# Performance work log

Hardware: AMD Instinct MI355X
Metric: run time of the kernel (lower is better)

## Reference

```python
import jax, jax.numpy as jnp
import numpy as np

N_SRC = 50000
N_DST = 50000
N_EDGES = 1_600_000
D_NEIGH = 128
D_SELF = 128
D_EDGE = 32
D_OUT = 256


def setup_inputs() -> dict:
    key = jax.random.key(0)
    k = jax.random.split(key, 7)
    h_neigh = jax.random.normal(k[0], (N_SRC, D_NEIGH), dtype=jnp.float32)
    h_self = jax.random.normal(k[1], (N_DST, D_SELF), dtype=jnp.float32)
    edge_feats = jax.random.normal(k[2], (N_EDGES, D_EDGE), dtype=jnp.float32)
    src = jax.random.randint(k[3], (N_EDGES,), 0, N_SRC, dtype=jnp.int32)
    dst = jax.random.randint(k[4], (N_EDGES,), 0, N_DST, dtype=jnp.int32)
    # xavier-ish small weights
    W_self = jax.random.normal(k[5], (D_OUT, D_SELF), dtype=jnp.float32) * 0.05
    W_neigh = jax.random.normal(k[6], (D_OUT, D_NEIGH + D_EDGE), dtype=jnp.float32) * 0.05
    return {"h_neigh": h_neigh, "h_self": h_self, "edge_feats": edge_feats,
            "src": src, "dst": dst, "W_self": W_self, "W_neigh": W_neigh}


def reference(h_neigh, h_self, edge_feats, src, dst, W_self, W_neigh):
    n_dst = h_self.shape[0]
    # in-degree per destination node (mean denominator); zero-degree -> 0 result like DGL
    deg = jax.ops.segment_sum(jnp.ones_like(dst, dtype=h_neigh.dtype), dst, num_segments=n_dst)
    denom = jnp.where(deg == 0, 1.0, deg)[:, None]
    # fn.copy_e + mean: mean of edge features per destination node
    edge_agg = jax.ops.segment_sum(edge_feats, dst, num_segments=n_dst) / denom  # [n_dst, D_EDGE]
    # fn.copy_u + mean: gather neighbor features along edges, mean-scatter to dst
    neigh_agg = jax.ops.segment_sum(h_neigh[src], dst, num_segments=n_dst) / denom  # [n_dst, D_NEIGH]
    hn = jnp.concatenate([neigh_agg, edge_agg], axis=1)  # [n_dst, D_NEIGH+D_EDGE]
    z = jax.nn.relu(h_self @ W_self.T + hn @ W_neigh.T)  # [n_dst, D_OUT]
    z_norm = jnp.linalg.norm(z, ord=2, axis=1, keepdims=True)
    z_norm = jnp.where(z_norm == 0, 1.0, z_norm)
    return z / z_norm
```

## Files before the change

kernel.cpp:

```cpp
#include <hip/hip_runtime.h>

#define N_SRC 50000
#define N_DST 50000
#define N_EDGES 1600000
#define D_NEIGH 128
#define D_SELF 128
#define D_EDGE 32
#define D_OUT 256
#define K_TOT 288
#define D_HN 160

#define NB 196
#define CPAD 16
#define CHUNK 2048
#define CAPSH 14
#define NSCAT1 256

typedef float f32x4 __attribute__((ext_vector_type(4)));
typedef short s16x8 __attribute__((ext_vector_type(8)));
typedef float fv4 __attribute__((ext_vector_type(4)));
typedef float fv2 __attribute__((ext_vector_type(2)));
typedef unsigned short uv4 __attribute__((ext_vector_type(4)));

__device__ __forceinline__ ushort f2bf(float x) {
    unsigned b = __float_as_uint(x);
    return (ushort)((b + 0x7fffu + ((b >> 16) & 1u)) >> 16);
}
__device__ __forceinline__ float bflo(unsigned u) { return __uint_as_float(u << 16); }
__device__ __forceinline__ float bfhi(unsigned u) { return __uint_as_float(u & 0xffff0000u); }


#if defined(__has_builtin)
#if __has_builtin(__builtin_amdgcn_cvt_pk_fp8_f32) && __has_builtin(__builtin_amdgcn_cvt_pk_f32_fp8)
#define FP8_HW 1
#endif
#endif

__device__ __forceinline__ unsigned enc_fp8_scalar(float x) {
    unsigned b = __float_as_uint(x);
    const unsigned s = b >> 31;
    float ax = fabsf(x);
    ax = fminf(ax, 448.f);
    if (ax < 0.015625f) return s << 7;
    unsigned ab = __float_as_uint(ax);
    unsigned lsb = (ab >> 20) & 1u;
    unsigned b2 = ab + 0x7FFFFu + lsb;
    unsigned e = ((b2 >> 23) & 0xFFu) - 120u;
    unsigned m = (b2 >> 20) & 7u;
    if (e > 15u) { e = 15u; m = 6u; }
    return (s << 7) | (e << 3) | m;
}

__device__ __forceinline__ unsigned enc_fp8x4(float4 f) {
#ifdef FP8_HW
    int r = 0;
    r = __builtin_amdgcn_cvt_pk_fp8_f32(f.x, f.y, r, false);
    r = __builtin_amdgcn_cvt_pk_fp8_f32(f.z, f.w, r, true);
    return (unsigned)r;
#else
    return enc_fp8_scalar(f.x) | (enc_fp8_scalar(f.y) << 8) |
           (enc_fp8_scalar(f.z) << 16) | (enc_fp8_scalar(f.w) << 24);
#endif
}

__device__ __forceinline__ float dec_fp8_scalar(unsigned u) {
    unsigned e = (u >> 3) & 15u;
    unsigned bits = ((u & 0x80u) << 24) | (((u & 0x7Fu) << 20) + (120u << 23));
    return (e == 0) ? 0.f : __uint_as_float(bits);
}

__device__ __forceinline__ void dec_fp8x4(unsigned u, float* f) {
#ifdef FP8_HW
    fv2 lo = __builtin_amdgcn_cvt_pk_f32_fp8(u, false);
    fv2 hi = __builtin_amdgcn_cvt_pk_f32_fp8(u, true);
    f[0] = lo.x; f[1] = lo.y; f[2] = hi.x; f[3] = hi.y;
#else
    f[0] = dec_fp8_scalar(u);
    f[1] = dec_fp8_scalar(u >> 8);
    f[2] = dec_fp8_scalar(u >> 16);
    f[3] = dec_fp8_scalar(u >> 24);
#endif
}


__global__ __launch_bounds__(256) void k_pre(const int* __restrict__ dst,
                                             const int* __restrict__ src,
                                             int* __restrict__ gcur0,
                                             int2* __restrict__ pk1,
                                             const float* __restrict__ h_neigh,
                                             unsigned* __restrict__ hb,
                                             const float* __restrict__ Wself,
                                             const float* __restrict__ Wneigh,
                                             ushort* __restrict__ Wb) {
    __shared__ int hist[NB];
    __shared__ int lbase[NB];
    __shared__ int gbase[NB];
    __shared__ int2 stage[CHUNK];
    const int blk = blockIdx.x;
    const int tid = threadIdx.x;

    if (blk >= NSCAT1) {
        const int bb = blk - NSCAT1;
        if (bb < 6250) {
            const int i = bb * 256 + tid;
            float4 f = ((const float4*)h_neigh)[i];
            hb[i] = enc_fp8x4(f);
        } else {
            const int q = (bb - 6250) * 256 + tid;
            if (q >= 9 * 4 * 256) return;
            const int t = q >> 10;
            const int r = q & 1023;
            const int k8 = r >> 8;
            const int c = r & 255;
            const int kb = t * 32 + k8 * 8;
            const float* p = (kb < 128) ? (Wself + (size_t)c * D_SELF + kb)
                                        : (Wneigh + (size_t)c * D_HN + (kb - 128));
            float4 f0 = *(const float4*)(p);
            float4 f1 = *(const float4*)(p + 4);
            ushort* o = Wb + (size_t)q * 8;
            *(ushort4*)(o)     = make_ushort4(f2bf(f0.x), f2bf(f0.y), f2bf(f0.z), f2bf(f0.w));
            *(ushort4*)(o + 4) = make_ushort4(f2bf(f1.x), f2bf(f1.y), f2bf(f1.z), f2bf(f1.w));
        }
        return;
    }

    const int n = N_EDGES;
    for (int c0 = blk * CHUNK; c0 < n; c0 += NSCAT1 * CHUNK) {
        const int m = min(CHUNK, n - c0);
        for (int t = tid; t < NB; t += 256) hist[t] = 0;
        __syncthreads();
        int d8[8], s8[8];
#pragma unroll
        for (int j = 0; j < 8; j++) {
            const int i = c0 + j * 256 + tid;
            if (i < n) { d8[j] = dst[i]; s8[j] = src[i]; atomicAdd(&hist[d8[j] >> 8], 1); }
        }
        __syncthreads();
        if (tid == 0) {
            int ex = 0;
            for (int b = 0; b < NB; b++) { lbase[b] = ex; ex += hist[b]; }
        }
        __syncthreads();
        for (int t = tid; t < NB; t += 256)
            gbase[t] = hist[t] ? atomicAdd(&gcur0[t * CPAD], hist[t]) : 0;
        __syncthreads();
        for (int t = tid; t < NB; t += 256) hist[t] = lbase[t];
        __syncthreads();
#pragma unroll
        for (int j = 0; j < 8; j++) {
            const int i = c0 + j * 256 + tid;
            if (i < n) {
                const unsigned cb = (unsigned)d8[j] >> 8;
                const int p = atomicAdd(&hist[cb], 1);
                stage[p] = make_int2(i, (int)((unsigned)s8[j] |
                                              (((unsigned)d8[j] & 255u) << 16) | (cb << 24)));
            }
        }
        __syncthreads();
        for (int t = tid; t < m; t += 256) {
            int2 v = stage[t];
            const int cb = (v.y >> 24) & 255;
            v.y &= 0x00FFFFFF;
            pk1[((size_t)cb << CAPSH) + gbase[cb] + (t - lbase[cb])] = v;
        }
        __syncthreads();
    }
}


__global__ __launch_bounds__(1024) void k_scat2(const int* __restrict__ gcur0,
                                                const int2* __restrict__ pk1,
                                                int2* __restrict__ pk2,
                                                int2* __restrict__ rs2) {
    __shared__ int part[256];
    __shared__ int cur[256];
    const int b = blockIdx.x;
    const int n = gcur0[b * CPAD];
    const int base = b << CAPSH;
    const int tid = threadIdx.x;
    if (tid < 256) part[tid] = 0;
    __syncthreads();
    for (int i = tid; i < n; i += 1024)
        atomicAdd(&part[(pk1[base + i].y >> 16) & 255], 1);
    __syncthreads();
    const int c0 = (tid < 256) ? part[tid] : 0;
    __syncthreads();
    for (int off = 1; off < 256; off <<= 1) {
        int v = 0;
        if (tid < 256 && tid >= off) v = part[tid - off];
        __syncthreads();
        if (tid < 256) part[tid] += v;
        __syncthreads();
    }
    if (tid < 256) {
        const int pfx = part[tid] - c0;
        cur[tid] = pfx;
        const int gn = b * 256 + tid;
        if (gn < N_DST) rs2[gn] = make_int2(base + pfx, base + pfx + c0);
    }
    __syncthreads();
    for (int i = tid; i < n; i += 1024) {
        int2 v = pk1[base + i];
        const int dl = (v.y >> 16) & 255;
        const int p = atomicAdd(&cur[dl], 1);
        pk2[base + p] = make_int2(v.x, v.y & 0xFFFF);
    }
}


__global__ void k_cvtall(const float* __restrict__ in, unsigned* __restrict__ hb,
                         const float* __restrict__ Wself, const float* __restrict__ Wneigh,
                         ushort* __restrict__ Wb) {
    const int b = blockIdx.x;
    if (b < 6250) {
        const int i = b * 256 + threadIdx.x;
        float4 f = ((const float4*)in)[i];
        hb[i] = enc_fp8x4(f);
    } else {
        const int q = (b - 6250) * 256 + threadIdx.x;
        if (q >= 9 * 4 * 256) return;
        const int t = q >> 10;
        const int r = q & 1023;
        const int k8 = r >> 8;
        const int c = r & 255;
        const int kb = t * 32 + k8 * 8;
        const float* p = (kb < 128) ? (Wself + (size_t)c * D_SELF + kb)
                                    : (Wneigh + (size_t)c * D_HN + (kb - 128));
        float4 f0 = *(const float4*)(p);
        float4 f1 = *(const float4*)(p + 4);
        ushort* o = Wb + (size_t)q * 8;
        *(ushort4*)(o)     = make_ushort4(f2bf(f0.x), f2bf(f0.y), f2bf(f0.z), f2bf(f0.w));
        *(ushort4*)(o + 4) = make_ushort4(f2bf(f1.x), f2bf(f1.y), f2bf(f1.z), f2bf(f1.w));
    }
}

__global__ void k_deg(const int* __restrict__ dst, int* __restrict__ deg, int n) {
    int i = blockIdx.x * blockDim.x + threadIdx.x;
    if (i < n) atomicAdd(&deg[dst[i]], 1);
}

__global__ __launch_bounds__(1024) void k_scan(const int* __restrict__ deg,
                                               int* __restrict__ row_start,
                                               int* __restrict__ cursor) {
    __shared__ int part[1024];
    const int t = threadIdx.x;
    const int CH = (N_DST + 1023) / 1024;
    const int b = t * CH;
    int s = 0;
    for (int i = 0; i < CH; i++) { int idx = b + i; if (idx < N_DST) s += deg[idx]; }
    part[t] = s;
    __syncthreads();
    for (int off = 1; off < 1024; off <<= 1) {
        int v = (t >= off) ? part[t - off] : 0;
        __syncthreads();
        part[t] += v;
        __syncthreads();
    }
    int ex = (t == 0) ? 0 : part[t - 1];
    for (int i = 0; i < CH; i++) {
        int idx = b + i;
        if (idx < N_DST) { row_start[idx] = ex; cursor[idx] = ex; ex += deg[idx]; }
    }
    if (t == 1023) row_start[N_DST] = part[1023];
}

__global__ void k_fill(const int* __restrict__ dst, const int* __restrict__ src,
                       int* __restrict__ cursor, int2* __restrict__ pk, int n) {
    int i = blockIdx.x * blockDim.x + threadIdx.x;
    if (i < n) {
        int p = atomicAdd(&cursor[dst[i]], 1);
        pk[p] = make_int2(i, src[i]);
    }
}

__global__ void k_mkrs2(const int* __restrict__ row_start, int2* __restrict__ rs2) {
    int i = blockIdx.x * blockDim.x + threadIdx.x;
    if (i < N_DST) rs2[i] = make_int2(row_start[i], row_start[i + 1]);
}


__global__ __launch_bounds__(64) void k_agg(const int2* __restrict__ rs2,
                                            const int2* __restrict__ pk,
                                            const unsigned char* __restrict__ hb,
                                            const float* __restrict__ ef,
                                            ushort* __restrict__ hnb) {
    const int d = blockIdx.x;
    const int lane = threadIdx.x;
    const int ll = lane & 31;
    const int g = lane >> 5;
    const int2 se = rs2[d];
    const int start = se.x, end = se.y;
    const int deg = end - start;
    float a0 = 0.f, a1 = 0.f, a2 = 0.f, a3 = 0.f, ae = 0.f;
    const unsigned char* hbase = hb + 4 * ll;
    const float* ebase = ef + ll;

    for (int c = start; c < end; c += 64) {
        const int rem = end - c;
        const int m = rem < 64 ? rem : 64;
        int e = 0, s = 0;
        if (lane < m) {
            unsigned long long pv =
                __builtin_nontemporal_load((const unsigned long long*)&pk[c + lane]);
            e = (int)(unsigned)pv;
            s = (int)(unsigned)(pv >> 32);
        }
        int i = 0;
        for (; i + 16 <= m; i += 16) {
            unsigned u[8];
            float te[8];
#pragma unroll
            for (int j = 0; j < 8; j++) {
                const int sj = __shfl(s, i + 2 * j + g);
                u[j] = *(const unsigned*)(hbase + (size_t)sj * D_NEIGH);
            }
#pragma unroll
            for (int j = 0; j < 8; j++) {
                const int ee = __shfl(e, i + 2 * j + g);
                te[j] = __builtin_nontemporal_load(ebase + (size_t)ee * D_EDGE);
            }
#pragma unroll
            for (int j = 0; j < 8; j++) {
                float f[4];
                dec_fp8x4(u[j], f);
                a0 += f[0]; a1 += f[1]; a2 += f[2]; a3 += f[3];
                ae += te[j];
            }
        }
        for (; i + 8 <= m; i += 8) {
            unsigned u[4];
            float te[4];
#pragma unroll
            for (int j = 0; j < 4; j++) {
                const int sj = __shfl(s, i + 2 * j + g);
                u[j] = *(const unsigned*)(hbase + (size_t)sj * D_NEIGH);
            }
#pragma unroll
            for (int j = 0; j < 4; j++) {
                const int ee = __shfl(e, i + 2 * j + g);
                te[j] = __builtin_nontemporal_load(ebase + (size_t)ee * D_EDGE);
            }
#pragma unroll
            for (int j = 0; j < 4; j++) {
                float f[4];
                dec_fp8x4(u[j], f);
                a0 += f[0]; a1 += f[1]; a2 += f[2]; a3 += f[3];
                ae += te[j];
            }
        }
        for (; i < m; ++i) {
            const int si = __builtin_amdgcn_readlane(s, i);
            const int ei = __builtin_amdgcn_readlane(e, i);
            if (g == 0) {
                const unsigned uu = *(const unsigned*)(hbase + (size_t)si * D_NEIGH);
                float f[4];
                dec_fp8x4(uu, f);
                a0 += f[0]; a1 += f[1]; a2 += f[2]; a3 += f[3];
                ae += __builtin_nontemporal_load(ebase + (size_t)ei * D_EDGE);
            }
        }
    }

    a0 += __shfl_xor(a0, 32); a1 += __shfl_xor(a1, 32);
    a2 += __shfl_xor(a2, 32); a3 += __shfl_xor(a3, 32);
    ae += __shfl_xor(ae, 32);

    if (lane < 32) {
        const float inv = 1.0f / (float)(deg > 0 ? deg : 1);
        ushort* o = hnb + (size_t)d * D_HN;
        *(ushort4*)(o + 4 * ll) = make_ushort4(f2bf(a0 * inv), f2bf(a1 * inv),
                                               f2bf(a2 * inv), f2bf(a3 * inv));
        o[128 + ll] = f2bf(ae * inv);
    }
}


#define GBM 128

__global__ __launch_bounds__(512) void k_gemm_norm(const float* __restrict__ h_self,
                                                   const ushort* __restrict__ hnb,
                                                   const ushort* __restrict__ Wb,
                                                   float* __restrict__ out) {
    __shared__ __align__(16) ushort Xs[2][GBM * 40];
    __shared__ float rsum[2][GBM];
    __shared__ float invn[GBM];

    const int tid = threadIdx.x;
    const int lane = tid & 63;
    const int wid = tid >> 6;
    const int wm = wid >> 1;
    const int wn = wid & 1;
    const int brow = blockIdx.x * GBM;
    const int xrow = tid >> 2, xpart = tid & 3;
    const int koff8 = lane >> 4, rsel = lane & 15;

    f32x4 acc[2][8] = {};

    auto stageX = [&](int t, int bufi) {
        const int k0 = t * 32;
        const int gr = brow + xrow;
        uv4 v0 = (uv4)0, v1 = (uv4)0;
        if (gr < N_DST) {
            if (k0 < 128) {
                const float* sp = h_self + (size_t)gr * D_SELF + k0 + xpart * 8;
                fv4 f0 = __builtin_nontemporal_load((const fv4*)(sp));
                fv4 f1 = __builtin_nontemporal_load((const fv4*)(sp + 4));
                v0 = (uv4){f2bf(f0.x), f2bf(f0.y), f2bf(f0.z), f2bf(f0.w)};
                v1 = (uv4){f2bf(f1.x), f2bf(f1.y), f2bf(f1.z), f2bf(f1.w)};
            } else {
                const ushort* sp = hnb + (size_t)gr * D_HN + (k0 - 128) + xpart * 8;
                v0 = __builtin_nontemporal_load((const uv4*)(sp));
                v1 = __builtin_nontemporal_load((const uv4*)(sp + 4));
            }
        }
        *(uv4*)&Xs[bufi][xrow * 40 + xpart * 8] = v0;
        *(uv4*)&Xs[bufi][xrow * 40 + xpart * 8 + 4] = v1;
    };

    stageX(0, 0);
    __syncthreads();

    for (int t = 0; t < 9; t++) {
        if (t < 8) stageX(t + 1, (t + 1) & 1);
        s16x8 af[2], bf[8];
#pragma unroll
        for (int fi = 0; fi < 2; fi++)
            af[fi] = *(const s16x8*)&Xs[t & 1][(wm * 32 + fi * 16 + rsel) * 40 + koff8 * 8];
#pragma unroll
        for (int fj = 0; fj < 8; fj++)
            bf[fj] = *(const s16x8*)&Wb[((size_t)(t * 4 + koff8) * 256 +
                                         (wn * 128 + fj * 16 + rsel)) * 8];
#pragma unroll
        for (int fi = 0; fi < 2; fi++)
#pragma unroll
            for (int fj = 0; fj < 8; fj++)
                acc[fi][fj] = __builtin_amdgcn_mfma_f32_16x16x32_bf16(af[fi], bf[fj], acc[fi][fj], 0, 0, 0);
        __syncthreads();
    }

    float ss[2][4];
#pragma unroll
    for (int fi = 0; fi < 2; fi++)
#pragma unroll
        for (int j = 0; j < 4; j++) {
            float s = 0.f;
#pragma unroll
            for (int fj = 0; fj < 8; fj++) {
                float z = fmaxf(acc[fi][fj][j], 0.f);
                acc[fi][fj][j] = z;
                s += z * z;
            }
            ss[fi][j] = s;
        }
#pragma unroll
    for (int m = 1; m < 16; m <<= 1)
#pragma unroll
        for (int fi = 0; fi < 2; fi++)
#pragma unroll
            for (int j = 0; j < 4; j++) ss[fi][j] += __shfl_xor(ss[fi][j], m);
    if ((lane & 15) == 0) {
        const int gg = lane >> 4;
#pragma unroll
        for (int fi = 0; fi < 2; fi++)
#pragma unroll
            for (int j = 0; j < 4; j++)
                rsum[wn][wm * 32 + fi * 16 + gg * 4 + j] = ss[fi][j];
    }
    __syncthreads();
    if (tid < GBM) {
        float t = rsum[0][tid] + rsum[1][tid];
        invn[tid] = (t > 0.f) ? 1.f / sqrtf(t) : 1.f;
    }
    __syncthreads();

#pragma unroll
    for (int fi = 0; fi < 2; fi++)
#pragma unroll
        for (int j = 0; j < 4; j++) {
            const int rl = wm * 32 + fi * 16 + (lane >> 4) * 4 + j;
            const int row = brow + rl;
            if (row < N_DST) {
                const float iv = invn[rl];
#pragma unroll
                for (int fj = 0; fj < 8; fj++)
                    __builtin_nontemporal_store(acc[fi][fj][j] * iv,
                        &out[(size_t)row * D_OUT + wn * 128 + fj * 16 + (lane & 15)]);
            }
        }
}


extern "C" void kernel_launch(void* const* d_in, const int* in_sizes, int n_in,
                              void* d_out, int out_size, void* d_ws, size_t ws_size,
                              hipStream_t stream) {
    const float* h_neigh = (const float*)d_in[0];
    const float* h_self  = (const float*)d_in[1];
    const float* ef      = (const float*)d_in[2];
    const int*   src     = (const int*)d_in[3];
    const int*   dst     = (const int*)d_in[4];
    const float* Wself   = (const float*)d_in[5];
    const float* Wneigh  = (const float*)d_in[6];
    float* out = (float*)d_out;

    char* ws = (char*)d_ws;
    const size_t PKB = (size_t)NB << CAPSH;
    const size_t need_new = 524288ull + 2 * PKB * 8 + 12800000ull + 16000000ull + 147456ull;

    if (ws_size >= need_new) {
        int*   gcur0 = (int*)(ws + 0);
        int2*  rs2   = (int2*)(ws + 16384);
        int2*  pk1   = (int2*)(ws + 524288);
        int2*  pk2   = (int2*)(ws + 524288 + PKB * 8);
        unsigned* hb = (unsigned*)(ws + 524288 + 2 * PKB * 8);
        ushort* hnb  = (ushort*)((char*)hb + 12800000);
        ushort* Wb   = (ushort*)((char*)hnb + 16000000);

        hipMemsetAsync(gcur0, 0, NB * CPAD * sizeof(int), stream);
        k_pre<<<NSCAT1 + 6250 + 36, 256, 0, stream>>>(dst, src, gcur0, pk1,
                                                      h_neigh, hb, Wself, Wneigh, Wb);
        k_scat2<<<NB, 1024, 0, stream>>>(gcur0, pk1, pk2, rs2);
        k_agg<<<N_DST, 64, 0, stream>>>(rs2, pk2, (const unsigned char*)hb, ef, hnb);
        k_gemm_norm<<<(N_DST + GBM - 1) / GBM, 512, 0, stream>>>(h_self, hnb, Wb, out);
    } else {
        int* deg       = (int*)(ws + 0);
        int* row_start = (int*)(ws + 262144);
        int* cursor    = (int*)(ws + 524288);
        int2* pk       = (int2*)(ws + 786432);
        unsigned* hb   = (unsigned*)(ws + 13586432);
        ushort* hnb    = (ushort*)(ws + 26386432);
        ushort* Wb     = (ushort*)(ws + 42386432);
        int2* rs2      = (int2*)(ws + 42533888);

        hipMemsetAsync(deg, 0, N_DST * sizeof(int), stream);
        k_cvtall<<<6286, 256, 0, stream>>>(h_neigh, hb, Wself, Wneigh, Wb);
        k_deg<<<(N_EDGES + 255) / 256, 256, 0, stream>>>(dst, deg, N_EDGES);
        k_scan<<<1, 1024, 0, stream>>>(deg, row_start, cursor);
        k_fill<<<(N_EDGES + 255) / 256, 256, 0, stream>>>(dst, src, cursor, pk, N_EDGES);
        k_mkrs2<<<(N_DST + 255) / 256, 256, 0, stream>>>(row_start, rs2);
        k_agg<<<N_DST, 64, 0, stream>>>(rs2, pk, (const unsigned char*)hb, ef, hnb);
        k_gemm_norm<<<(N_DST + GBM - 1) / GBM, 512, 0, stream>>>(h_self, hnb, Wb, out);
    }
}
```

Before: 151.1 us.

## Fuse second scatter pass into aggregation with 64-node buckets sorted in LDS

After: 163.8 us. +8.4%, slower.

```diff
diff --git a/kernel.cpp b/kernel.cpp
--- a/kernel.cpp
+++ b/kernel.cpp
@@ -10,10 +10,10 @@
 #define K_TOT 288
 #define D_HN 160
 
-#define NB 196
+#define NBF 782
 #define CPAD 16
 #define CHUNK 2048
-#define CAPSH 14
+#define CAPSH 12
 #define NSCAT1 256
 
 typedef float f32x4 __attribute__((ext_vector_type(4)));
@@ -26,8 +26,6 @@
     unsigned b = __float_as_uint(x);
     return (ushort)((b + 0x7fffu + ((b >> 16) & 1u)) >> 16);
 }
-__device__ __forceinline__ float bflo(unsigned u) { return __uint_as_float(u << 16); }
-__device__ __forceinline__ float bfhi(unsigned u) { return __uint_as_float(u & 0xffff0000u); }
 
 
 #if defined(__has_builtin)
@@ -89,12 +87,15 @@
                                              int2* __restrict__ pk1,
                                              const float* __restrict__ h_neigh,
                                              unsigned* __restrict__ hb,
+                                             const float* __restrict__ h_self,
+                                             ushort* __restrict__ hsb,
                                              const float* __restrict__ Wself,
                                              const float* __restrict__ Wneigh,
                                              ushort* __restrict__ Wb) {
-    __shared__ int hist[NB];
-    __shared__ int lbase[NB];
-    __shared__ int gbase[NB];
+    __shared__ int hist[NBF];
+    __shared__ int lbase[NBF];
+    __shared__ int gbase[NBF];
+    __shared__ int partial[256];
     __shared__ int2 stage[CHUNK];
     const int blk = blockIdx.x;
     const int tid = threadIdx.x;
@@ -105,8 +106,12 @@
             const int i = bb * 256 + tid;
             float4 f = ((const float4*)h_neigh)[i];
             hb[i] = enc_fp8x4(f);
+        } else if (bb < 12500) {
+            const int i = (bb - 6250) * 256 + tid;
+            float4 f = ((const float4*)h_self)[i];
+            ((ushort4*)hsb)[i] = make_ushort4(f2bf(f.x), f2bf(f.y), f2bf(f.z), f2bf(f.w));
         } else {
-            const int q = (bb - 6250) * 256 + tid;
+            const int q = (bb - 12500) * 256 + tid;
             if (q >= 9 * 4 * 256) return;
             const int t = q >> 10;
             const int r = q & 1023;
@@ -127,40 +132,58 @@
     const int n = N_EDGES;
     for (int c0 = blk * CHUNK; c0 < n; c0 += NSCAT1 * CHUNK) {
         const int m = min(CHUNK, n - c0);
-        for (int t = tid; t < NB; t += 256) hist[t] = 0;
+        for (int t = tid; t < NBF; t += 256) hist[t] = 0;
         __syncthreads();
         int d8[8], s8[8];
 #pragma unroll
         for (int j = 0; j < 8; j++) {
             const int i = c0 + j * 256 + tid;
-            if (i < n) { d8[j] = dst[i]; s8[j] = src[i]; atomicAdd(&hist[d8[j] >> 8], 1); }
-        }
-        __syncthreads();
-        if (tid == 0) {
-            int ex = 0;
-            for (int b = 0; b < NB; b++) { lbase[b] = ex; ex += hist[b]; }
-        }
-        __syncthreads();
-        for (int t = tid; t < NB; t += 256)
+            if (i < n) { d8[j] = dst[i]; s8[j] = src[i]; atomicAdd(&hist[d8[j] >> 6], 1); }
+        }
+        __syncthreads();
+        int loc[4];
+        int sum = 0;
+#pragma unroll
+        for (int j = 0; j < 4; j++) {
+            const int bi = tid * 4 + j;
+            loc[j] = (bi < NBF) ? hist[bi] : 0;
+            sum += loc[j];
+        }
+        partial[tid] = sum;
+        __syncthreads();
+        for (int off = 1; off < 256; off <<= 1) {
+            int v = (tid >= off) ? partial[tid - off] : 0;
+            __syncthreads();
+            partial[tid] += v;
+            __syncthreads();
+        }
+        int ex = (tid == 0) ? 0 : partial[tid - 1];
+#pragma unroll
+        for (int j = 0; j < 4; j++) {
+            const int bi = tid * 4 + j;
+            if (bi < NBF) { lbase[bi] = ex; ex += loc[j]; }
+        }
+        __syncthreads();
+        for (int t = tid; t < NBF; t += 256)
             gbase[t] = hist[t] ? atomicAdd(&gcur0[t * CPAD], hist[t]) : 0;
         __syncthreads();
-        for (int t = tid; t < NB; t += 256) hist[t] = lbase[t];
+        for (int t = tid; t < NBF; t += 256) hist[t] = lbase[t];
         __syncthreads();
 #pragma unroll
         for (int j = 0; j < 8; j++) {
             const int i = c0 + j * 256 + tid;
             if (i < n) {
-                const unsigned cb = (unsigned)d8[j] >> 8;
+                const unsigned cb = (unsigned)d8[j] >> 6;
                 const int p = atomicAdd(&hist[cb], 1);
                 stage[p] = make_int2(i, (int)((unsigned)s8[j] |
-                                              (((unsigned)d8[j] & 255u) << 16) | (cb << 24)));
+                                              (((unsigned)d8[j] & 63u) << 16) | (cb << 22)));
             }
         }
         __syncthreads();
         for (int t = tid; t < m; t += 256) {
             int2 v = stage[t];
-            const int cb = (v.y >> 24) & 255;
-            v.y &= 0x00FFFFFF;
+            const unsigned cb = ((unsigned)v.y >> 22) & 1023u;
+            v.y &= 0x3FFFFF;
             pk1[((size_t)cb << CAPSH) + gbase[cb] + (t - lbase[cb])] = v;
         }
         __syncthreads();
@@ -168,216 +191,151 @@
 }
 
 
-__global__ __launch_bounds__(1024) void k_scat2(const int* __restrict__ gcur0,
-                                                const int2* __restrict__ pk1,
-                                                int2* __restrict__ pk2,
-                                                int2* __restrict__ rs2) {
-    __shared__ int part[256];
-    __shared__ int cur[256];
+__global__ __launch_bounds__(512) void k_aggs2(const int* __restrict__ gcur0,
+                                               const int2* __restrict__ pk1,
+                                               const unsigned char* __restrict__ hb,
+                                               const float* __restrict__ ef,
+                                               ushort* __restrict__ hnb) {
+    __shared__ int2 sorted[1 << CAPSH];
+    __shared__ int h[64];
+    __shared__ int sbase[65];
+    __shared__ int cur[64];
     const int b = blockIdx.x;
-    const int n = gcur0[b * CPAD];
-    const int base = b << CAPSH;
     const int tid = threadIdx.x;
-    if (tid < 256) part[tid] = 0;
-    __syncthreads();
-    for (int i = tid; i < n; i += 1024)
-        atomicAdd(&part[(pk1[base + i].y >> 16) & 255], 1);
-    __syncthreads();
-    const int c0 = (tid < 256) ? part[tid] : 0;
-    __syncthreads();
-    for (int off = 1; off < 256; off <<= 1) {
-        int v = 0;
-        if (tid < 256 && tid >= off) v = part[tid - off];
-        __syncthreads();
-        if (tid < 256) part[tid] += v;
-        __syncthreads();
-    }
-    if (tid < 256) {
-        const int pfx = part[tid] - c0;
-        cur[tid] = pfx;
-        const int gn = b * 256 + tid;
-        if (gn < N_DST) rs2[gn] = make_int2(base + pfx, base + pfx + c0);
-    }
-    __syncthreads();
-    for (int i = tid; i < n; i += 1024) {
-        int2 v = pk1[base + i];
-        const int dl = (v.y >> 16) & 255;
+    const int lane = tid & 63;
+    const int wid = tid >> 6;
+    const int nn = min(gcur0[b * CPAD], 1 << CAPSH);
+    const size_t base = (size_t)b << CAPSH;
+
+    if (tid < 64) h[tid] = 0;
+    __syncthreads();
+
+    int2 ent[8];
+    int ne = 0;
+#pragma unroll
+    for (int j = 0; j < 8; j++) {
+        const int idx = j * 512 + tid;
+        if (idx < nn) {
+            unsigned long long pv =
+                __builtin_nontemporal_load((const unsigned long long*)&pk1[base + idx]);
+            ent[ne].x = (int)(unsigned)pv;
+            ent[ne].y = (int)(unsigned)(pv >> 32);
+            atomicAdd(&h[(ent[ne].y >> 16) & 63], 1);
+            ne++;
+        }
+    }
+    __syncthreads();
+    if (tid < 64) {
+        const int v = h[tid];
+        int p = v;
+#pragma unroll
+        for (int off = 1; off < 64; off <<= 1) {
+            int q = __shfl_up(p, off);
+            if (lane >= off) p += q;
+        }
+        sbase[tid + 1] = p;
+        if (tid == 0) sbase[0] = 0;
+        cur[tid] = p - v;
+    }
+    __syncthreads();
+    for (int j = 0; j < ne; j++) {
+        const int dl = (ent[j].y >> 16) & 63;
         const int p = atomicAdd(&cur[dl], 1);
-        pk2[base + p] = make_int2(v.x, v.y & 0xFFFF);
-    }
-}
-
-
-__global__ void k_cvtall(const float* __restrict__ in, unsigned* __restrict__ hb,
-                         const float* __restrict__ Wself, const float* __restrict__ Wneigh,
-                         ushort* __restrict__ Wb) {
-    const int b = blockIdx.x;
-    if (b < 6250) {
-        const int i = b * 256 + threadIdx.x;
-        float4 f = ((const float4*)in)[i];
-        hb[i] = enc_fp8x4(f);
-    } else {
-        const int q = (b - 6250) * 256 + threadIdx.x;
-        if (q >= 9 * 4 * 256) return;
-        const int t = q >> 10;
-        const int r = q & 1023;
-        const int k8 = r >> 8;
-        const int c = r & 255;
-        const int kb = t * 32 + k8 * 8;
-        const float* p = (kb < 128) ? (Wself + (size_t)c * D_SELF + kb)
-                                    : (Wneigh + (size_t)c * D_HN + (kb - 128));
-        float4 f0 = *(const float4*)(p);
-        float4 f1 = *(const float4*)(p + 4);
-        ushort* o = Wb + (size_t)q * 8;
-        *(ushort4*)(o)     = make_ushort4(f2bf(f0.x), f2bf(f0.y), f2bf(f0.z), f2bf(f0.w));
-        *(ushort4*)(o + 4) = make_ushort4(f2bf(f1.x), f2bf(f1.y), f2bf(f1.z), f2bf(f1.w));
-    }
-}
-
-__global__ void k_deg(const int* __restrict__ dst, int* __restrict__ deg, int n) {
-    int i = blockIdx.x * blockDim.x + threadIdx.x;
-    if (i < n) atomicAdd(&deg[dst[i]], 1);
-}
-
-__global__ __launch_bounds__(1024) void k_scan(const int* __restrict__ deg,
-                                               int* __restrict__ row_start,
-                                               int* __restrict__ cursor) {
-    __shared__ int part[1024];
-    const int t = threadIdx.x;
-    const int CH = (N_DST + 1023) / 1024;
-    const int b = t * CH;
-    int s = 0;
-    for (int i = 0; i < CH; i++) { int idx = b + i; if (idx < N_DST) s += deg[idx]; }
-    part[t] = s;
-    __syncthreads();
-    for (int off = 1; off < 1024; off <<= 1) {
-        int v = (t >= off) ? part[t - off] : 0;
-        __syncthreads();
-        part[t] += v;
-        __syncthreads();
-    }
-    int ex = (t == 0) ? 0 : part[t - 1];
-    for (int i = 0; i < CH; i++) {
-        int idx = b + i;
-        if (idx < N_DST) { row_start[idx] = ex; cursor[idx] = ex; ex += deg[idx]; }
-    }
-    if (t == 1023) row_start[N_DST] = part[1023];
-}
-
-__global__ void k_fill(const int* __restrict__ dst, const int* __restrict__ src,
-                       int* __restrict__ cursor, int2* __restrict__ pk, int n) {
-    int i = blockIdx.x * blockDim.x + threadIdx.x;
-    if (i < n) {
-        int p = atomicAdd(&cursor[dst[i]], 1);
-        pk[p] = make_int2(i, src[i]);
-    }
-}
-
-__global__ void k_mkrs2(const int* __restrict__ row_start, int2* __restrict__ rs2) {
-    int i = blockIdx.x * blockDim.x + threadIdx.x;
-    if (i < N_DST) rs2[i] = make_int2(row_start[i], row_start[i + 1]);
-}
-
-
-__global__ __launch_bounds__(64) void k_agg(const int2* __restrict__ rs2,
-                                            const int2* __restrict__ pk,
-                                            const unsigned char* __restrict__ hb,
-                                            const float* __restrict__ ef,
-                                            ushort* __restrict__ hnb) {
-    const int d = blockIdx.x;
-    const int lane = threadIdx.x;
+        sorted[p] = make_int2(ent[j].x, ent[j].y & 0xFFFF);
+    }
+    __syncthreads();
+
+    const int g = lane >> 5;
     const int ll = lane & 31;
-    const int g = lane >> 5;
-    const int2 se = rs2[d];
-    const int start = se.x, end = se.y;
-    const int deg = end - start;
-    float a0 = 0.f, a1 = 0.f, a2 = 0.f, a3 = 0.f, ae = 0.f;
     const unsigned char* hbase = hb + 4 * ll;
     const float* ebase = ef + ll;
 
-    for (int c = start; c < end; c += 64) {
-        const int rem = end - c;
-        const int m = rem < 64 ? rem : 64;
-        int e = 0, s = 0;
-        if (lane < m) {
-            unsigned long long pv =
-                __builtin_nontemporal_load((const unsigned long long*)&pk[c + lane]);
-            e = (int)(unsigned)pv;
-            s = (int)(unsigned)(pv >> 32);
-        }
-        int i = 0;
-        for (; i + 16 <= m; i += 16) {
-            unsigned u[8];
-            float te[8];
-#pragma unroll
-            for (int j = 0; j < 8; j++) {
-                const int sj = __shfl(s, i + 2 * j + g);
-                u[j] = *(const unsigned*)(hbase + (size_t)sj * D_NEIGH);
-            }
-#pragma unroll
-            for (int j = 0; j < 8; j++) {
-                const int ee = __shfl(e, i + 2 * j + g);
-                te[j] = __builtin_nontemporal_load(ebase + (size_t)ee * D_EDGE);
-            }
-#pragma unroll
-            for (int j = 0; j < 8; j++) {
-                float f[4];
-                dec_fp8x4(u[j], f);
-                a0 += f[0]; a1 += f[1]; a2 += f[2]; a3 += f[3];
-                ae += te[j];
-            }
-        }
-        for (; i + 8 <= m; i += 8) {
-            unsigned u[4];
-            float te[4];
-#pragma unroll
-            for (int j = 0; j < 4; j++) {
-                const int sj = __shfl(s, i + 2 * j + g);
-                u[j] = *(const unsigned*)(hbase + (size_t)sj * D_NEIGH);
-            }
-#pragma unroll
-            for (int j = 0; j < 4; j++) {
-                const int ee = __shfl(e, i + 2 * j + g);
-                te[j] = __builtin_nontemporal_load(ebase + (size_t)ee * D_EDGE);
-            }
-#pragma unroll
-            for (int j = 0; j < 4; j++) {
-                float f[4];
-                dec_fp8x4(u[j], f);
-                a0 += f[0]; a1 += f[1]; a2 += f[2]; a3 += f[3];
-                ae += te[j];
-            }
-        }
-        for (; i < m; ++i) {
-            const int si = __builtin_amdgcn_readlane(s, i);
-            const int ei = __builtin_amdgcn_readlane(e, i);
-            if (g == 0) {
-                const unsigned uu = *(const unsigned*)(hbase + (size_t)si * D_NEIGH);
-                float f[4];
-                dec_fp8x4(uu, f);
-                a0 += f[0]; a1 += f[1]; a2 += f[2]; a3 += f[3];
-                ae += __builtin_nontemporal_load(ebase + (size_t)ei * D_EDGE);
-            }
-        }
-    }
-
-    a0 += __shfl_xor(a0, 32); a1 += __shfl_xor(a1, 32);
-    a2 += __shfl_xor(a2, 32); a3 += __shfl_xor(a3, 32);
-    ae += __shfl_xor(ae, 32);
-
-    if (lane < 32) {
-        const float inv = 1.0f / (float)(deg > 0 ? deg : 1);
-        ushort* o = hnb + (size_t)d * D_HN;
-        *(ushort4*)(o + 4 * ll) = make_ushort4(f2bf(a0 * inv), f2bf(a1 * inv),
-                                               f2bf(a2 * inv), f2bf(a3 * inv));
-        o[128 + ll] = f2bf(ae * inv);
+    for (int r = 0; r < 8; r++) {
+        const int dl = wid * 8 + r;
+        const int gn = b * 64 + dl;
+        const int start = sbase[dl], end = sbase[dl + 1];
+        const int deg = end - start;
+        float a0 = 0.f, a1 = 0.f, a2 = 0.f, a3 = 0.f, ae = 0.f;
+
+        for (int c = start; c < end; c += 64) {
+            const int rem = end - c;
+            const int m = rem < 64 ? rem : 64;
+            int e = 0, s = 0;
+            if (lane < m) { int2 p = sorted[c + lane]; e = p.x; s = p.y; }
+            int i = 0;
+            for (; i + 16 <= m; i += 16) {
+                unsigned u[8];
+                float te[8];
+#pragma unroll
+                for (int j = 0; j < 8; j++) {
+                    const int sj = __shfl(s, i + 2 * j + g);
+                    u[j] = *(const unsigned*)(hbase + (size_t)sj * D_NEIGH);
+                }
+#pragma unroll
+                for (int j = 0; j < 8; j++) {
+                    const int ee = __shfl(e, i + 2 * j + g);
+                    te[j] = __builtin_nontemporal_load(ebase + (size_t)ee * D_EDGE);
+                }
+#pragma unroll
+                for (int j = 0; j < 8; j++) {
+                    float f[4];
+                    dec_fp8x4(u[j], f);
+                    a0 += f[0]; a1 += f[1]; a2 += f[2]; a3 += f[3];
+                    ae += te[j];
+                }
+            }
+            for (; i + 8 <= m; i += 8) {
+                unsigned u[4];
+                float te[4];
+#pragma unroll
+                for (int j = 0; j < 4; j++) {
+                    const int sj = __shfl(s, i + 2 * j + g);
+                    u[j] = *(const unsigned*)(hbase + (size_t)sj * D_NEIGH);
+                }
+#pragma unroll
+                for (int j = 0; j < 4; j++) {
+                    const int ee = __shfl(e, i + 2 * j + g);
+                    te[j] = __builtin_nontemporal_load(ebase + (size_t)ee * D_EDGE);
+                }
+#pragma unroll
+                for (int j = 0; j < 4; j++) {
+                    float f[4];
+                    dec_fp8x4(u[j], f);
+                    a0 += f[0]; a1 += f[1]; a2 += f[2]; a3 += f[3];
+                    ae += te[j];
+                }
+            }
+            for (; i < m; ++i) {
+                const int si = __builtin_amdgcn_readlane(s, i);
+                const int ei = __builtin_amdgcn_readlane(e, i);
+                if (g == 0) {
+                    const unsigned uu = *(const unsigned*)(hbase + (size_t)si * D_NEIGH);
+                    float f[4];
+                    dec_fp8x4(uu, f);
+                    a0 += f[0]; a1 += f[1]; a2 += f[2]; a3 += f[3];
+                    ae += __builtin_nontemporal_load(ebase + (size_t)ei * D_EDGE);
+                }
+            }
+        }
+
+        a0 += __shfl_xor(a0, 32); a1 += __shfl_xor(a1, 32);
+        a2 += __shfl_xor(a2, 32); a3 += __shfl_xor(a3, 32);
+        ae += __shfl_xor(ae, 32);
+
+        if (gn < N_DST && lane < 32) {
+            const float inv = 1.0f / (float)(deg > 0 ? deg : 1);
+            ushort* o = hnb + (size_t)gn * D_HN;
+            *(ushort4*)(o + 4 * ll) = make_ushort4(f2bf(a0 * inv), f2bf(a1 * inv),
+                                                   f2bf(a2 * inv), f2bf(a3 * inv));
+            o[128 + ll] = f2bf(ae * inv);
+        }
     }
 }
 
 
 #define GBM 128
 
-__global__ __launch_bounds__(512) void k_gemm_norm(const float* __restrict__ h_self,
+__global__ __launch_bounds__(512) void k_gemm_norm(const ushort* __restrict__ hsb,
                                                    const ushort* __restrict__ hnb,
                                                    const ushort* __restrict__ Wb,
                                                    float* __restrict__ out) {
@@ -401,17 +359,10 @@
         const int gr = brow + xrow;
         uv4 v0 = (uv4)0, v1 = (uv4)0;
         if (gr < N_DST) {
-            if (k0 < 128) {
-                const float* sp = h_self + (size_t)gr * D_SELF + k0 + xpart * 8;
-                fv4 f0 = __builtin_nontemporal_load((const fv4*)(sp));
-                fv4 f1 = __builtin_nontemporal_load((const fv4*)(sp + 4));
-                v0 = (uv4){f2bf(f0.x), f2bf(f0.y), f2bf(f0.z), f2bf(f0.w)};
-                v1 = (uv4){f2bf(f1.x), f2bf(f1.y), f2bf(f1.z), f2bf(f1.w)};
-            } else {
-                const ushort* sp = hnb + (size_t)gr * D_HN + (k0 - 128) + xpart * 8;
-                v0 = __builtin_nontemporal_load((const uv4*)(sp));
-                v1 = __builtin_nontemporal_load((const uv4*)(sp + 4));
-            }
+            const ushort* sp = (k0 < 128) ? (hsb + (size_t)gr * D_SELF + k0 + xpart * 8)
+                                          : (hnb + (size_t)gr * D_HN + (k0 - 128) + xpart * 8);
+            v0 = __builtin_nontemporal_load((const uv4*)(sp));
+            v1 = __builtin_nontemporal_load((const uv4*)(sp + 4));
         }
         *(uv4*)&Xs[bufi][xrow * 40 + xpart * 8] = v0;
         *(uv4*)&Xs[bufi][xrow * 40 + xpart * 8 + 4] = v1;
@@ -503,41 +454,17 @@
     float* out = (float*)d_out;
 
     char* ws = (char*)d_ws;
-    const size_t PKB = (size_t)NB << CAPSH;
-    const size_t need_new = 524288ull + 2 * PKB * 8 + 12800000ull + 16000000ull + 147456ull;
-
-    if (ws_size >= need_new) {
-        int*   gcur0 = (int*)(ws + 0);
-        int2*  rs2   = (int2*)(ws + 16384);
-        int2*  pk1   = (int2*)(ws + 524288);
-        int2*  pk2   = (int2*)(ws + 524288 + PKB * 8);
-        unsigned* hb = (unsigned*)(ws + 524288 + 2 * PKB * 8);
-        ushort* hnb  = (ushort*)((char*)hb + 12800000);
-        ushort* Wb   = (ushort*)((char*)hnb + 16000000);
-
-        hipMemsetAsync(gcur0, 0, NB * CPAD * sizeof(int), stream);
-        k_pre<<<NSCAT1 + 6250 + 36, 256, 0, stream>>>(dst, src, gcur0, pk1,
-                                                      h_neigh, hb, Wself, Wneigh, Wb);
-        k_scat2<<<NB, 1024, 0, stream>>>(gcur0, pk1, pk2, rs2);
-        k_agg<<<N_DST, 64, 0, stream>>>(rs2, pk2, (const unsigned char*)hb, ef, hnb);
-        k_gemm_norm<<<(N_DST + GBM - 1) / GBM, 512, 0, stream>>>(h_self, hnb, Wb, out);
-    } else {
-        int* deg       = (int*)(ws + 0);
-        int* row_start = (int*)(ws + 262144);
-        int* cursor    = (int*)(ws + 524288);
-        int2* pk       = (int2*)(ws + 786432);
-        unsigned* hb   = (unsigned*)(ws + 13586432);
-        ushort* hnb    = (ushort*)(ws + 26386432);
-        ushort* Wb     = (ushort*)(ws + 42386432);
-        int2* rs2      = (int2*)(ws + 42533888);
-
-        hipMemsetAsync(deg, 0, N_DST * sizeof(int), stream);
-        k_cvtall<<<6286, 256, 0, stream>>>(h_neigh, hb, Wself, Wneigh, Wb);
-        k_deg<<<(N_EDGES + 255) / 256, 256, 0, stream>>>(dst, deg, N_EDGES);
-        k_scan<<<1, 1024, 0, stream>>>(deg, row_start, cursor);
-        k_fill<<<(N_EDGES + 255) / 256, 256, 0, stream>>>(dst, src, cursor, pk, N_EDGES);
-        k_mkrs2<<<(N_DST + 255) / 256, 256, 0, stream>>>(row_start, rs2);
-        k_agg<<<N_DST, 64, 0, stream>>>(rs2, pk, (const unsigned char*)hb, ef, hnb);
-        k_gemm_norm<<<(N_DST + GBM - 1) / GBM, 512, 0, stream>>>(h_self, hnb, Wb, out);
-    }
-}
+    int*      gcur0 = (int*)(ws + 0);
+    int2*     pk1   = (int2*)(ws + 65536);
+    unsigned* hb    = (unsigned*)(ws + 25690112);
+    ushort*   hsb   = (ushort*)(ws + 32090112);
+    ushort*   hnb   = (ushort*)(ws + 44890112);
+    ushort*   Wb    = (ushort*)(ws + 60890112);
+
+    hipMemsetAsync(gcur0, 0, NBF * CPAD * sizeof(int), stream);
+    k_pre<<<NSCAT1 + 6250 + 6250 + 36, 256, 0, stream>>>(dst, src, gcur0, pk1,
+                                                         h_neigh, hb, h_self, hsb,
+                                                         Wself, Wneigh, Wb);
+    k_aggs2<<<NBF, 512, 0, stream>>>(gcur0, pk1, (const unsigned char*)hb, ef, hnb);
+    k_gemm_norm<<<(N_DST + GBM - 1) / GBM, 512, 0, stream>>>(hsb, hnb, Wb, out);
+}
```
